# Performance work log

Hardware: AMD Instinct MI355X
Metric: run time of the kernel (lower is better)

Reference implementation:

```python
import jax, jax.numpy as jnp
import numpy as np

N_U, N_I, D, Q, NNZ, L = 100000, 100000, 64, 128, 3200000, 3
N = N_U + N_I

def setup_inputs() -> dict:
    key = jax.random.key(0)
    ks = jax.random.split(key, 9)
    user_emb = jax.random.normal(ks[0], (N_U, D), dtype=jnp.float32) * 0.1
    item_emb = jax.random.normal(ks[1], (N_I, D), dtype=jnp.float32) * 0.1
    adj_row = jax.random.randint(ks[2], (NNZ,), 0, N, dtype=jnp.int32)
    adj_col = jax.random.randint(ks[3], (NNZ,), 0, N, dtype=jnp.int32)
    # ~degree-normalized values so L-layer propagation stays stable
    adj_vals = jax.random.uniform(ks[4], (NNZ,), dtype=jnp.float32) / 16.0
    ut = jax.random.normal(ks[5], (Q, N_U), dtype=jnp.float32) * (1.0 / np.sqrt(N_U))
    vt = jax.random.normal(ks[6], (Q, N_I), dtype=jnp.float32) * (1.0 / np.sqrt(N_I))
    u_mul_s = jax.random.normal(ks[7], (N_U, Q), dtype=jnp.float32) * 0.1
    v_mul_s = jax.random.normal(ks[8], (N_I, Q), dtype=jnp.float32) * 0.1
    return {"user_emb": user_emb, "item_emb": item_emb, "adj_row": adj_row,
            "adj_col": adj_col, "adj_vals": adj_vals, "ut": ut, "vt": vt,
            "u_mul_s": u_mul_s, "v_mul_s": v_mul_s}

def _spmm(row, col, vals, x):
    # y[r] = sum_{e: row[e]==r} vals[e] * x[col[e]]
    return jax.ops.segment_sum(vals[:, None] * x[col], row, num_segments=N)

def reference(user_emb, item_emb, adj_row, adj_col, adj_vals, ut, vt, u_mul_s, v_mul_s):
    ego = jnp.concatenate([user_emb, item_emb], axis=0)  # [N, D]
    acc = jnp.zeros_like(ego)
    svd_u = jnp.zeros((N_U, D), dtype=ego.dtype)
    svd_i = jnp.zeros((N_I, D), dtype=ego.dtype)
    for _ in range(L):
        ego = _spmm(adj_row, adj_col, adj_vals, ego)
        acc = acc + ego
        ue, ie = ego[:N_U], ego[N_U:]
        ut_eu = ut @ ue            # [Q, D]
        vt_ei = vt @ ie            # [Q, D]
        svd_u = svd_u + u_mul_s @ vt_ei
        svd_i = svd_i + v_mul_s @ ut_eu
    mean = acc / L                 # mean over stacked layer embeddings
    return (mean[:N_U], svd_u, mean[N_U:], svd_i)
```

## Files before the change

kernel.cpp:

```cpp
#include <hip/hip_runtime.h>

constexpr int N_U  = 100000;
constexpr int N_I  = 100000;
constexpr int NTOT = 200000;
constexpr int D    = 64;
constexpr int Q    = 128;
constexpr int NNZ  = 3200000;
constexpr int SEG  = N_U * D;

constexpr int G1_CHUNK = 400;
constexpr int G1_NBLK  = 250;

constexpr int BROWS   = 512;
constexpr int NBUCK   = (NTOT + BROWS - 1) / BROWS;
constexpr int P_CHUNK = 8192;
constexpr int P_NBLK  = (NNZ + P_CHUNK - 1) / P_CHUNK;

constexpr int G2_ROWS = 64;
constexpr int G2_NBLK = (N_U + G2_ROWS - 1) / G2_ROWS;

__device__ __forceinline__ unsigned short f2bf(float f) {
  unsigned int b = __float_as_uint(f);
  return (unsigned short)((b + 0x7fff + ((b >> 16) & 1)) >> 16);
}
__device__ __forceinline__ float bf2f(unsigned short u) {
  return __uint_as_float((unsigned int)u << 16);
}

__global__ void __launch_bounds__(512) k_bhist(const int* __restrict__ row,
                                               int* __restrict__ part) {
  __shared__ int h[NBUCK];
  const int t = threadIdx.x;
  if (t < NBUCK) h[t] = 0;
  __syncthreads();
  const int e0 = blockIdx.x * P_CHUNK;
#pragma unroll
  for (int i = 0; i < P_CHUNK / 512; ++i) {
    int e = e0 + i * 512 + t;
    if (e < NNZ) atomicAdd(&h[row[e] >> 9], 1);
  }
  __syncthreads();
  if (t < NBUCK) part[blockIdx.x * NBUCK + t] = h[t];
}

__global__ void __launch_bounds__(512) k_bscan(int* __restrict__ part,
                                               int* __restrict__ outb,
                                               int* __restrict__ bbase) {
  __shared__ int s[512];
  const int t = threadIdx.x;
  int run = 0;
  if (t < NBUCK) {
    for (int blk = 0; blk < P_NBLK; ++blk) {
      int v = part[blk * NBUCK + t];
      outb[blk * NBUCK + t] = run;
      run += v;
    }
  }
  const int own = (t < NBUCK) ? run : 0;
  s[t] = own;
  __syncthreads();
  for (int off = 1; off < 512; off <<= 1) {
    int y = (t >= off) ? s[t - off] : 0;
    __syncthreads();
    s[t] += y;
    __syncthreads();
  }
  int excl = s[t] - own;
  if (t <= NBUCK) bbase[t] = excl;
}

__global__ void __launch_bounds__(512) k_mscat(const int* __restrict__ row,
                                               const int* __restrict__ col,
                                               const float* __restrict__ val,
                                               const int* __restrict__ outb,
                                               const int* __restrict__ bbase,
                                               int2* __restrict__ ebuck) {
  __shared__ int cur[NBUCK];
  const int t = threadIdx.x;
  if (t < NBUCK) cur[t] = bbase[t] + outb[blockIdx.x * NBUCK + t];
  __syncthreads();
  const int e0 = blockIdx.x * P_CHUNK;
#pragma unroll
  for (int i = 0; i < P_CHUNK / 512; ++i) {
    int e = e0 + i * 512 + t;
    if (e < NNZ) {
      int r = row[e];
      int b = r >> 9;
      int pos = atomicAdd(&cur[b], 1);
      ebuck[pos] = make_int2(col[e] | ((r & (BROWS - 1)) << 18), __float_as_int(val[e]));
    }
  }
}

__global__ void __launch_bounds__(512) k_rsort(const int* __restrict__ bbase,
                                               const int2* __restrict__ ebuck,
                                               int2* __restrict__ edges,
                                               int* __restrict__ rowptr) {
  __shared__ int s[512];
  __shared__ int cur[512];
  const int t = threadIdx.x;
  const int b = blockIdx.x;
  const int eb0 = bbase[b], eb1 = bbase[b + 1];
  cur[t] = 0;
  __syncthreads();
  for (int e = eb0 + t; e < eb1; e += 512) atomicAdd(&cur[ebuck[e].x >> 18], 1);
  __syncthreads();
  const int own = cur[t];
  s[t] = own;
  __syncthreads();
  for (int off = 1; off < 512; off <<= 1) {
    int y = (t >= off) ? s[t - off] : 0;
    __syncthreads();
    s[t] += y;
    __syncthreads();
  }
  const int excl = s[t] - own;
  const int r = (b << 9) + t;
  if (r < NTOT) rowptr[r] = eb0 + excl;
  if (b == NBUCK - 1 && t == 0) rowptr[NTOT] = NNZ;
  cur[t] = eb0 + excl;
  __syncthreads();
  for (int e = eb0 + t; e < eb1; e += 512) {
    int2 kv = ebuck[e];
    int pos = atomicAdd(&cur[kv.x >> 18], 1);
    edges[pos] = make_int2(kv.x & 0x3FFFF, kv.y);
  }
}

__global__ void k_cvt(const float* __restrict__ user_emb,
                      const float* __restrict__ item_emb,
                      unsigned short* __restrict__ e0) {
  int i = blockIdx.x * 256 + threadIdx.x;
  if (i >= NTOT * D / 8) return;
  size_t base = (size_t)i * 8;
  const float* src = (base < (size_t)SEG) ? (user_emb + base) : (item_emb + base - SEG);
  float4 v0 = *reinterpret_cast<const float4*>(src);
  float4 v1 = *reinterpret_cast<const float4*>(src + 4);
  union { unsigned short us[8]; uint4 u4; } pk;
  pk.us[0] = f2bf(v0.x); pk.us[1] = f2bf(v0.y); pk.us[2] = f2bf(v0.z); pk.us[3] = f2bf(v0.w);
  pk.us[4] = f2bf(v1.x); pk.us[5] = f2bf(v1.y); pk.us[6] = f2bf(v1.z); pk.us[7] = f2bf(v1.w);
  *reinterpret_cast<uint4*>(e0 + base) = pk.u4;
}

__global__ void k_spmm(const int* __restrict__ rowptr, const int2* __restrict__ edges,
                       const unsigned short* __restrict__ src,
                       unsigned short* __restrict__ dst) {
  const int r = (blockIdx.x * 256 + threadIdx.x) >> 6;
  const int lane = threadIdx.x & 63;
  if (r >= NTOT) return;
  const int e0 = rowptr[r], e1 = rowptr[r + 1];
  float sum = 0.f;
  int e = e0;
  for (; e + 8 <= e1; e += 8) {
    int2 d0 = edges[e + 0], d1 = edges[e + 1], d2 = edges[e + 2], d3 = edges[e + 3];
    int2 d4 = edges[e + 4], d5 = edges[e + 5], d6 = edges[e + 6], d7 = edges[e + 7];
    unsigned short u0 = src[((size_t)d0.x << 6) + lane];
    unsigned short u1 = src[((size_t)d1.x << 6) + lane];
    unsigned short u2 = src[((size_t)d2.x << 6) + lane];
    unsigned short u3 = src[((size_t)d3.x << 6) + lane];
    unsigned short u4 = src[((size_t)d4.x << 6) + lane];
    unsigned short u5 = src[((size_t)d5.x << 6) + lane];
    unsigned short u6 = src[((size_t)d6.x << 6) + lane];
    unsigned short u7 = src[((size_t)d7.x << 6) + lane];
    sum = fmaf(__int_as_float(d0.y), bf2f(u0), sum);
    sum = fmaf(__int_as_float(d1.y), bf2f(u1), sum);
    sum = fmaf(__int_as_float(d2.y), bf2f(u2), sum);
    sum = fmaf(__int_as_float(d3.y), bf2f(u3), sum);
    sum = fmaf(__int_as_float(d4.y), bf2f(u4), sum);
    sum = fmaf(__int_as_float(d5.y), bf2f(u5), sum);
    sum = fmaf(__int_as_float(d6.y), bf2f(u6), sum);
    sum = fmaf(__int_as_float(d7.y), bf2f(u7), sum);
  }
  for (; e + 2 <= e1; e += 2) {
    int2 d0 = edges[e + 0], d1 = edges[e + 1];
    unsigned short u0 = src[((size_t)d0.x << 6) + lane];
    unsigned short u1 = src[((size_t)d1.x << 6) + lane];
    sum = fmaf(__int_as_float(d0.y), bf2f(u0), sum);
    sum = fmaf(__int_as_float(d1.y), bf2f(u1), sum);
  }
  if (e < e1) {
    int2 d0 = edges[e];
    sum = fmaf(__int_as_float(d0.y), bf2f(src[((size_t)d0.x << 6) + lane]), sum);
  }
  dst[((size_t)r << 6) + lane] = f2bf(sum);
}

__global__ void k_mean(const unsigned short* __restrict__ e1,
                       const unsigned short* __restrict__ e2,
                       const unsigned short* __restrict__ e3,
                       float* __restrict__ mean_u, float* __restrict__ mean_i) {
  int i = blockIdx.x * 256 + threadIdx.x;
  if (i >= NTOT * D / 8) return;
  size_t base = (size_t)i * 8;
  uint4 a = *reinterpret_cast<const uint4*>(e1 + base);
  uint4 b = *reinterpret_cast<const uint4*>(e2 + base);
  uint4 c = *reinterpret_cast<const uint4*>(e3 + base);
  union { uint4 u4; unsigned short us[8]; } ua, ub, uc;
  ua.u4 = a; ub.u4 = b; uc.u4 = c;
  float o[8];
#pragma unroll
  for (int j = 0; j < 8; ++j)
    o[j] = (bf2f(ua.us[j]) + bf2f(ub.us[j]) + bf2f(uc.us[j])) * (1.f / 3.f);
  float* dstp = (base < (size_t)SEG) ? (mean_u + base) : (mean_i + base - SEG);
  *reinterpret_cast<float4*>(dstp) = make_float4(o[0], o[1], o[2], o[3]);
  *reinterpret_cast<float4*>(dstp + 4) = make_float4(o[4], o[5], o[6], o[7]);
}

__global__ void __launch_bounds__(512) k_g1(const float* __restrict__ ut,
                                            const float* __restrict__ vt,
                                            const float* __restrict__ accu,
                                            const float* __restrict__ acci,
                                            float* __restrict__ Ppart) {
  __shared__ float Wl[128 * 65];
  __shared__ float Xl[64 * 64];
  const int mat = blockIdx.y;
  const float* __restrict__ W = mat ? vt : ut;
  const float* __restrict__ X = mat ? acci : accu;
  const int t = threadIdx.x;
  const int q0 = (t >> 4) * 4;
  const int d0 = (t & 15) * 4;
  const int n0 = blockIdx.x * G1_CHUNK;
  const int n1 = min(n0 + G1_CHUNK, N_U);
  float4 a0 = {0, 0, 0, 0}, a1 = {0, 0, 0, 0}, a2 = {0, 0, 0, 0}, a3 = {0, 0, 0, 0};
  for (int k = n0; k < n1; k += 64) {
#pragma unroll
    for (int rep = 0; rep < 2; ++rep) {
      int f4 = t + rep * 512;
      int row = f4 >> 4;
      int c4 = (f4 & 15) * 4;
      int gr = k + row;
      float4 v = (gr < n1) ? *reinterpret_cast<const float4*>(X + (size_t)gr * 64 + c4)
                           : float4{0, 0, 0, 0};
      *reinterpret_cast<float4*>(&Xl[row * 64 + c4]) = v;
    }
    {
      int q = t >> 2;
      int c16 = (t & 3) * 16;
#pragma unroll
      for (int jj = 0; jj < 4; ++jj) {
        int kk = c16 + jj * 4;
        int gk = k + kk;
        float4 v = (gk < n1) ? *reinterpret_cast<const float4*>(W + (size_t)q * N_U + gk)
                             : float4{0, 0, 0, 0};
        *reinterpret_cast<float4*>(&Wl[q * 65 + kk]) = v;
      }
    }
    __syncthreads();
#pragma unroll 2
    for (int kk = 0; kk < 64; kk += 4) {
      float4 w0 = *reinterpret_cast<const float4*>(&Wl[(q0 + 0) * 65 + kk]);
      float4 w1 = *reinterpret_cast<const float4*>(&Wl[(q0 + 1) * 65 + kk]);
      float4 w2 = *reinterpret_cast<const float4*>(&Wl[(q0 + 2) * 65 + kk]);
      float4 w3 = *reinterpret_cast<const float4*>(&Wl[(q0 + 3) * 65 + kk]);
      float4 x0 = *reinterpret_cast<const float4*>(&Xl[(kk + 0) * 64 + d0]);
      float4 x1 = *reinterpret_cast<const float4*>(&Xl[(kk + 1) * 64 + d0]);
      float4 x2 = *reinterpret_cast<const float4*>(&Xl[(kk + 2) * 64 + d0]);
      float4 x3 = *reinterpret_cast<const float4*>(&Xl[(kk + 3) * 64 + d0]);
#define FMA16(aj, wj)                                                                 \
  aj.x = fmaf(wj.x, x0.x, aj.x); aj.y = fmaf(wj.x, x0.y, aj.y);                       \
  aj.z = fmaf(wj.x, x0.z, aj.z); aj.w = fmaf(wj.x, x0.w, aj.w);                       \
  aj.x = fmaf(wj.y, x1.x, aj.x); aj.y = fmaf(wj.y, x1.y, aj.y);                       \
  aj.z = fmaf(wj.y, x1.z, aj.z); aj.w = fmaf(wj.y, x1.w, aj.w);                       \
  aj.x = fmaf(wj.z, x2.x, aj.x); aj.y = fmaf(wj.z, x2.y, aj.y);                       \
  aj.z = fmaf(wj.z, x2.z, aj.z); aj.w = fmaf(wj.z, x2.w, aj.w);                       \
  aj.x = fmaf(wj.w, x3.x, aj.x); aj.y = fmaf(wj.w, x3.y, aj.y);                       \
  aj.z = fmaf(wj.w, x3.z, aj.z); aj.w = fmaf(wj.w, x3.w, aj.w);
      FMA16(a0, w0)
      FMA16(a1, w1)
      FMA16(a2, w2)
      FMA16(a3, w3)
#undef FMA16
    }
    __syncthreads();
  }
  float* dst = Ppart + ((size_t)mat * G1_NBLK + blockIdx.x) * (Q * D);
  *reinterpret_cast<float4*>(dst + (q0 + 0) * 64 + d0) = a0;
  *reinterpret_cast<float4*>(dst + (q0 + 1) * 64 + d0) = a1;
  *reinterpret_cast<float4*>(dst + (q0 + 2) * 64 + d0) = a2;
  *reinterpret_cast<float4*>(dst + (q0 + 3) * 64 + d0) = a3;
}

__global__ void k_reduce(const float* __restrict__ Ppart, float* __restrict__ P) {
  int idx = blockIdx.x * 256 + threadIdx.x;
  if (idx >= 2 * Q * D) return;
  int mat = idx >> 13;
  int qd = idx & (Q * D - 1);
  const float* src = Ppart + (size_t)mat * G1_NBLK * (Q * D) + qd;
  float s = 0.f;
#pragma unroll 4
  for (int b = 0; b < G1_NBLK; ++b) s += src[(size_t)b * (Q * D)];
  P[idx] = s * 3.f;
}

__global__ void __launch_bounds__(256) k_g2(const float* __restrict__ u_mul_s,
                                            const float* __restrict__ v_mul_s,
                                            const float* __restrict__ P,
                                            float* __restrict__ svd_u,
                                            float* __restrict__ svd_i) {
  __shared__ float Pl[Q * D];
  const int mat = blockIdx.y;
  const float* __restrict__ M  = mat ? v_mul_s : u_mul_s;
  const float* __restrict__ Pg = mat ? P : (P + Q * D);
  float* __restrict__ outp     = mat ? svd_i : svd_u;
  const int t = threadIdx.x;
#pragma unroll
  for (int i = 0; i < 8; ++i) {
    int idx = i * 256 + t;
    reinterpret_cast<float4*>(Pl)[idx] = reinterpret_cast<const float4*>(Pg)[idx];
  }
  __syncthreads();
  const int c0 = (t & 15) * 4;
  const int rbase = blockIdx.x * G2_ROWS + (t >> 4) * 4;
  const float4* mr0 = reinterpret_cast<const float4*>(M + (size_t)(rbase + 0 < N_U ? rbase + 0 : 0) * Q);
  const float4* mr1 = reinterpret_cast<const float4*>(M + (size_t)(rbase + 1 < N_U ? rbase + 1 : 0) * Q);
  const float4* mr2 = reinterpret_cast<const float4*>(M + (size_t)(rbase + 2 < N_U ? rbase + 2 : 0) * Q);
  const float4* mr3 = reinterpret_cast<const float4*>(M + (size_t)(rbase + 3 < N_U ? rbase + 3 : 0) * Q);
  float4 a0 = {0, 0, 0, 0}, a1 = {0, 0, 0, 0}, a2 = {0, 0, 0, 0}, a3 = {0, 0, 0, 0};
#pragma unroll 4
  for (int k4 = 0; k4 < Q / 4; ++k4) {
    float4 m0 = mr0[k4];
    float4 m1 = mr1[k4];
    float4 m2 = mr2[k4];
    float4 m3 = mr3[k4];
    float4 p0 = *reinterpret_cast<const float4*>(&Pl[(k4 * 4 + 0) * D + c0]);
    float4 p1 = *reinterpret_cast<const float4*>(&Pl[(k4 * 4 + 1) * D + c0]);
    float4 p2 = *reinterpret_cast<const float4*>(&Pl[(k4 * 4 + 2) * D + c0]);
    float4 p3 = *reinterpret_cast<const float4*>(&Pl[(k4 * 4 + 3) * D + c0]);
#define G2FMA(aj, mj)                                                                 \
  aj.x = fmaf(mj.x, p0.x, aj.x); aj.y = fmaf(mj.x, p0.y, aj.y);                       \
  aj.z = fmaf(mj.x, p0.z, aj.z); aj.w = fmaf(mj.x, p0.w, aj.w);                       \
  aj.x = fmaf(mj.y, p1.x, aj.x); aj.y = fmaf(mj.y, p1.y, aj.y);                       \
  aj.z = fmaf(mj.y, p1.z, aj.z); aj.w = fmaf(mj.y, p1.w, aj.w);                       \
  aj.x = fmaf(mj.z, p2.x, aj.x); aj.y = fmaf(mj.z, p2.y, aj.y);                       \
  aj.z = fmaf(mj.z, p2.z, aj.z); aj.w = fmaf(mj.z, p2.w, aj.w);                       \
  aj.x = fmaf(mj.w, p3.x, aj.x); aj.y = fmaf(mj.w, p3.y, aj.y);                       \
  aj.z = fmaf(mj.w, p3.z, aj.z); aj.w = fmaf(mj.w, p3.w, aj.w);
    G2FMA(a0, m0)
    G2FMA(a1, m1)
    G2FMA(a2, m2)
    G2FMA(a3, m3)
#undef G2FMA
  }
  if (rbase + 0 < N_U) *reinterpret_cast<float4*>(outp + (size_t)(rbase + 0) * D + c0) = a0;
  if (rbase + 1 < N_U) *reinterpret_cast<float4*>(outp + (size_t)(rbase + 1) * D + c0) = a1;
  if (rbase + 2 < N_U) *reinterpret_cast<float4*>(outp + (size_t)(rbase + 2) * D + c0) = a2;
  if (rbase + 3 < N_U) *reinterpret_cast<float4*>(outp + (size_t)(rbase + 3) * D + c0) = a3;
}

extern "C" void kernel_launch(void* const* d_in, const int* in_sizes, int n_in,
                              void* d_out, int out_size, void* d_ws, size_t ws_size,
                              hipStream_t stream) {
  const float* user_emb = (const float*)d_in[0];
  const float* item_emb = (const float*)d_in[1];
  const int*   adj_row  = (const int*)d_in[2];
  const int*   adj_col  = (const int*)d_in[3];
  const float* adj_vals = (const float*)d_in[4];
  const float* ut       = (const float*)d_in[5];
  const float* vt       = (const float*)d_in[6];
  const float* u_mul_s  = (const float*)d_in[7];
  const float* v_mul_s  = (const float*)d_in[8];
  float* out = (float*)d_out;

  char* ws = (char*)d_ws;
  size_t off = 0;
  auto alloc = [&](size_t bytes) -> void* {
    void* p = ws + off;
    off = (off + bytes + 255) & ~(size_t)255;
    return p;
  };
  unsigned short* eb0 = (unsigned short*)alloc((size_t)NTOT * D * 2);
  unsigned short* eb1 = (unsigned short*)alloc((size_t)NTOT * D * 2);
  unsigned short* eb2 = (unsigned short*)alloc((size_t)NTOT * D * 2);
  unsigned short* eb3 = (unsigned short*)alloc((size_t)NTOT * D * 2);
  int2*  ebuck  = (int2*)alloc((size_t)NNZ * 8);
  int2*  edges  = (int2*)alloc((size_t)NNZ * 8);
  int*   rowptr = (int*)alloc((size_t)(NTOT + 1) * 4);
  int*   part   = (int*)alloc((size_t)P_NBLK * NBUCK * 4);
  int*   outb   = (int*)alloc((size_t)P_NBLK * NBUCK * 4);
  int*   bbase  = (int*)alloc((size_t)(NBUCK + 1) * 4);
  float* P      = (float*)alloc(2 * Q * D * 4);
  float* Ppart  = (float*)alloc((size_t)2 * G1_NBLK * Q * D * 4);

  float* mean_u = out;
  float* svd_u  = out + (size_t)SEG;
  float* mean_i = out + 2 * (size_t)SEG;
  float* svd_i  = out + 3 * (size_t)SEG;

  k_bhist<<<P_NBLK, 512, 0, stream>>>(adj_row, part);
  k_bscan<<<1, 512, 0, stream>>>(part, outb, bbase);
  k_mscat<<<P_NBLK, 512, 0, stream>>>(adj_row, adj_col, adj_vals, outb, bbase, ebuck);
  k_rsort<<<NBUCK, 512, 0, stream>>>(bbase, ebuck, edges, rowptr);

  k_cvt<<<(NTOT * D / 8 + 255) / 256, 256, 0, stream>>>(user_emb, item_emb, eb0);

  const int spmmGrid = (NTOT * 64) / 256;
  k_spmm<<<spmmGrid, 256, 0, stream>>>(rowptr, edges, eb0, eb1);
  k_spmm<<<spmmGrid, 256, 0, stream>>>(rowptr, edges, eb1, eb2);
  k_spmm<<<spmmGrid, 256, 0, stream>>>(rowptr, edges, eb2, eb3);

  k_mean<<<(NTOT * D / 8 + 255) / 256, 256, 0, stream>>>(eb1, eb2, eb3, mean_u, mean_i);

  k_g1<<<dim3(G1_NBLK, 2), 512, 0, stream>>>(ut, vt, mean_u, mean_i, Ppart);
  k_reduce<<<(2 * Q * D + 255) / 256, 256, 0, stream>>>(Ppart, P);

  k_g2<<<dim3(G2_NBLK, 2), 256, 0, stream>>>(u_mul_s, v_mul_s, P, svd_u, svd_i);
}
```

Before: 660.5 us.

## Fuse conversion into histogram, parallelize bucket scan, fold mean into last SpMM

The bf16 conversion of the embeddings now runs as extra blocks of the histogram kernel, which saves a launch. The serial per-bucket scan is split into a parallel wave-level scan per bucket plus a small global scan. The SpMM unrolls 16 edges with two accumulators, uses 32-bit indexing and nontemporal stores. The third layer computes the layer mean directly, so the separate mean kernel and one bf16 buffer are no longer needed. This cuts launch count and one full pass over the embeddings, at the cost of more register pressure in the SpMM.

```diff
diff --git a/kernel.cpp b/kernel.cpp
--- a/kernel.cpp
+++ b/kernel.cpp
@@ -19,6 +19,9 @@
 constexpr int G2_ROWS = 64;
 constexpr int G2_NBLK = (N_U + G2_ROWS - 1) / G2_ROWS;
 
+constexpr int CVT_CNT  = NTOT * D / 8;
+constexpr int CVT_BLKS = (CVT_CNT + 511) / 512;
+
 __device__ __forceinline__ unsigned short f2bf(float f) {
   unsigned int b = __float_as_uint(f);
   return (unsigned short)((b + 0x7fff + ((b >> 16) & 1)) >> 16);
@@ -27,36 +30,65 @@
   return __uint_as_float((unsigned int)u << 16);
 }
 
-__global__ void __launch_bounds__(512) k_bhist(const int* __restrict__ row,
-                                               int* __restrict__ part) {
+__global__ void __launch_bounds__(512) k_pre(const int* __restrict__ row,
+                                             int* __restrict__ part,
+                                             const float* __restrict__ user_emb,
+                                             const float* __restrict__ item_emb,
+                                             unsigned short* __restrict__ e0) {
   __shared__ int h[NBUCK];
   const int t = threadIdx.x;
-  if (t < NBUCK) h[t] = 0;
-  __syncthreads();
-  const int e0 = blockIdx.x * P_CHUNK;
-#pragma unroll
-  for (int i = 0; i < P_CHUNK / 512; ++i) {
-    int e = e0 + i * 512 + t;
-    if (e < NNZ) atomicAdd(&h[row[e] >> 9], 1);
-  }
-  __syncthreads();
-  if (t < NBUCK) part[blockIdx.x * NBUCK + t] = h[t];
-}
-
-__global__ void __launch_bounds__(512) k_bscan(int* __restrict__ part,
+  if (blockIdx.x < (unsigned)P_NBLK) {
+    if (t < NBUCK) h[t] = 0;
+    __syncthreads();
+    const int e0i = blockIdx.x * P_CHUNK;
+#pragma unroll
+    for (int i = 0; i < P_CHUNK / 512; ++i) {
+      int e = e0i + i * 512 + t;
+      if (e < NNZ) atomicAdd(&h[row[e] >> 9], 1);
+    }
+    __syncthreads();
+    if (t < NBUCK) part[blockIdx.x * NBUCK + t] = h[t];
+  } else {
+    int i = (blockIdx.x - P_NBLK) * 512 + t;
+    if (i >= CVT_CNT) return;
+    size_t base = (size_t)i * 8;
+    const float* src = (base < (size_t)SEG) ? (user_emb + base) : (item_emb + base - SEG);
+    float4 v0 = *reinterpret_cast<const float4*>(src);
+    float4 v1 = *reinterpret_cast<const float4*>(src + 4);
+    union { unsigned short us[8]; uint4 u4; } pk;
+    pk.us[0] = f2bf(v0.x); pk.us[1] = f2bf(v0.y); pk.us[2] = f2bf(v0.z); pk.us[3] = f2bf(v0.w);
+    pk.us[4] = f2bf(v1.x); pk.us[5] = f2bf(v1.y); pk.us[6] = f2bf(v1.z); pk.us[7] = f2bf(v1.w);
+    *reinterpret_cast<uint4*>(e0 + base) = pk.u4;
+  }
+}
+
+__global__ void __launch_bounds__(64) k_bscanA(const int* __restrict__ part,
                                                int* __restrict__ outb,
-                                               int* __restrict__ bbase) {
+                                               int* __restrict__ btot) {
+  const int b = blockIdx.x;
+  const int l = threadIdx.x;
+  int carry = 0;
+#pragma unroll
+  for (int round = 0; round < (P_NBLK + 63) / 64; ++round) {
+    int blk = round * 64 + l;
+    int v = (blk < P_NBLK) ? part[blk * NBUCK + b] : 0;
+    int x = v;
+#pragma unroll
+    for (int off = 1; off < 64; off <<= 1) {
+      int y = __shfl_up(x, off, 64);
+      if (l >= off) x += y;
+    }
+    if (blk < P_NBLK) outb[blk * NBUCK + b] = carry + x - v;
+    carry += __shfl(x, 63, 64);
+  }
+  if (l == 0) btot[b] = carry;
+}
+
+__global__ void __launch_bounds__(512) k_bscanB(const int* __restrict__ btot,
+                                                int* __restrict__ bbase) {
   __shared__ int s[512];
   const int t = threadIdx.x;
-  int run = 0;
-  if (t < NBUCK) {
-    for (int blk = 0; blk < P_NBLK; ++blk) {
-      int v = part[blk * NBUCK + t];
-      outb[blk * NBUCK + t] = run;
-      run += v;
-    }
-  }
-  const int own = (t < NBUCK) ? run : 0;
+  const int own = (t < NBUCK) ? btot[t] : 0;
   s[t] = own;
   __syncthreads();
   for (int off = 1; off < 512; off <<= 1) {
@@ -65,8 +97,7 @@
     s[t] += y;
     __syncthreads();
   }
-  int excl = s[t] - own;
-  if (t <= NBUCK) bbase[t] = excl;
+  if (t <= NBUCK) bbase[t] = s[t] - own;
 }
 
 __global__ void __launch_bounds__(512) k_mscat(const int* __restrict__ row,
@@ -127,83 +158,68 @@
   }
 }
 
-__global__ void k_cvt(const float* __restrict__ user_emb,
-                      const float* __restrict__ item_emb,
-                      unsigned short* __restrict__ e0) {
-  int i = blockIdx.x * 256 + threadIdx.x;
-  if (i >= NTOT * D / 8) return;
-  size_t base = (size_t)i * 8;
-  const float* src = (base < (size_t)SEG) ? (user_emb + base) : (item_emb + base - SEG);
-  float4 v0 = *reinterpret_cast<const float4*>(src);
-  float4 v1 = *reinterpret_cast<const float4*>(src + 4);
-  union { unsigned short us[8]; uint4 u4; } pk;
-  pk.us[0] = f2bf(v0.x); pk.us[1] = f2bf(v0.y); pk.us[2] = f2bf(v0.z); pk.us[3] = f2bf(v0.w);
-  pk.us[4] = f2bf(v1.x); pk.us[5] = f2bf(v1.y); pk.us[6] = f2bf(v1.z); pk.us[7] = f2bf(v1.w);
-  *reinterpret_cast<uint4*>(e0 + base) = pk.u4;
-}
-
+template <int FINAL>
 __global__ void k_spmm(const int* __restrict__ rowptr, const int2* __restrict__ edges,
                        const unsigned short* __restrict__ src,
-                       unsigned short* __restrict__ dst) {
+                       unsigned short* __restrict__ dst,
+                       const unsigned short* __restrict__ p1,
+                       const unsigned short* __restrict__ p2,
+                       float* __restrict__ mean_u, float* __restrict__ mean_i) {
   const int r = (blockIdx.x * 256 + threadIdx.x) >> 6;
   const int lane = threadIdx.x & 63;
   if (r >= NTOT) return;
-  const int e0 = rowptr[r], e1 = rowptr[r + 1];
-  float sum = 0.f;
-  int e = e0;
-  for (; e + 8 <= e1; e += 8) {
+  const int eb = rowptr[r], ee = rowptr[r + 1];
+  float sA = 0.f, sB = 0.f;
+  int e = eb;
+#define GIDX(dd) ((unsigned)(((dd).x << 6) + lane))
+  for (; e + 16 <= ee; e += 16) {
     int2 d0 = edges[e + 0], d1 = edges[e + 1], d2 = edges[e + 2], d3 = edges[e + 3];
     int2 d4 = edges[e + 4], d5 = edges[e + 5], d6 = edges[e + 6], d7 = edges[e + 7];
-    unsigned short u0 = src[((size_t)d0.x << 6) + lane];
-    unsigned short u1 = src[((size_t)d1.x << 6) + lane];
-    unsigned short u2 = src[((size_t)d2.x << 6) + lane];
-    unsigned short u3 = src[((size_t)d3.x << 6) + lane];
-    unsigned short u4 = src[((size_t)d4.x << 6) + lane];
-    unsigned short u5 = src[((size_t)d5.x << 6) + lane];
-    unsigned short u6 = src[((size_t)d6.x << 6) + lane];
-    unsigned short u7 = src[((size_t)d7.x << 6) + lane];
-    sum = fmaf(__int_as_float(d0.y), bf2f(u0), sum);
-    sum = fmaf(__int_as_float(d1.y), bf2f(u1), sum);
-    sum = fmaf(__int_as_float(d2.y), bf2f(u2), sum);
-    sum = fmaf(__int_as_float(d3.y), bf2f(u3), sum);
-    sum = fmaf(__int_as_float(d4.y), bf2f(u4), sum);
-    sum = fmaf(__int_as_float(d5.y), bf2f(u5), sum);
-    sum = fmaf(__int_as_float(d6.y), bf2f(u6), sum);
-    sum = fmaf(__int_as_float(d7.y), bf2f(u7), sum);
-  }
-  for (; e + 2 <= e1; e += 2) {
-    int2 d0 = edges[e + 0], d1 = edges[e + 1];
-    unsigned short u0 = src[((size_t)d0.x << 6) + lane];
-    unsigned short u1 = src[((size_t)d1.x << 6) + lane];
-    sum = fmaf(__int_as_float(d0.y), bf2f(u0), sum);
-    sum = fmaf(__int_as_float(d1.y), bf2f(u1), sum);
-  }
-  if (e < e1) {
+    int2 d8 = edges[e + 8], d9 = edges[e + 9], da = edges[e + 10], db = edges[e + 11];
+    int2 dc = edges[e + 12], dd = edges[e + 13], de = edges[e + 14], df = edges[e + 15];
+    unsigned short u0 = src[GIDX(d0)], u1 = src[GIDX(d1)], u2 = src[GIDX(d2)], u3 = src[GIDX(d3)];
+    unsigned short u4 = src[GIDX(d4)], u5 = src[GIDX(d5)], u6 = src[GIDX(d6)], u7 = src[GIDX(d7)];
+    unsigned short u8 = src[GIDX(d8)], u9 = src[GIDX(d9)], ua = src[GIDX(da)], ub = src[GIDX(db)];
+    unsigned short uc = src[GIDX(dc)], ud = src[GIDX(dd)], ue = src[GIDX(de)], uf = src[GIDX(df)];
+    sA = fmaf(__int_as_float(d0.y), bf2f(u0), sA);
+    sB = fmaf(__int_as_float(d1.y), bf2f(u1), sB);
+    sA = fmaf(__int_as_float(d2.y), bf2f(u2), sA);
+    sB = fmaf(__int_as_float(d3.y), bf2f(u3), sB);
+    sA = fmaf(__int_as_float(d4.y), bf2f(u4), sA);
+    sB = fmaf(__int_as_float(d5.y), bf2f(u5), sB);
+    sA = fmaf(__int_as_float(d6.y), bf2f(u6), sA);
+    sB = fmaf(__int_as_float(d7.y), bf2f(u7), sB);
+    sA = fmaf(__int_as_float(d8.y), bf2f(u8), sA);
+    sB = fmaf(__int_as_float(d9.y), bf2f(u9), sB);
+    sA = fmaf(__int_as_float(da.y), bf2f(ua), sA);
+    sB = fmaf(__int_as_float(db.y), bf2f(ub), sB);
+    sA = fmaf(__int_as_float(dc.y), bf2f(uc), sA);
+    sB = fmaf(__int_as_float(dd.y), bf2f(ud), sB);
+    sA = fmaf(__int_as_float(de.y), bf2f(ue), sA);
+    sB = fmaf(__int_as_float(df.y), bf2f(uf), sB);
+  }
+  for (; e + 4 <= ee; e += 4) {
+    int2 d0 = edges[e + 0], d1 = edges[e + 1], d2 = edges[e + 2], d3 = edges[e + 3];
+    unsigned short u0 = src[GIDX(d0)], u1 = src[GIDX(d1)], u2 = src[GIDX(d2)], u3 = src[GIDX(d3)];
+    sA = fmaf(__int_as_float(d0.y), bf2f(u0), sA);
+    sB = fmaf(__int_as_float(d1.y), bf2f(u1), sB);
+    sA = fmaf(__int_as_float(d2.y), bf2f(u2), sA);
+    sB = fmaf(__int_as_float(d3.y), bf2f(u3), sB);
+  }
+  for (; e < ee; ++e) {
     int2 d0 = edges[e];
-    sum = fmaf(__int_as_float(d0.y), bf2f(src[((size_t)d0.x << 6) + lane]), sum);
-  }
-  dst[((size_t)r << 6) + lane] = f2bf(sum);
-}
-
-__global__ void k_mean(const unsigned short* __restrict__ e1,
-                       const unsigned short* __restrict__ e2,
-                       const unsigned short* __restrict__ e3,
-                       float* __restrict__ mean_u, float* __restrict__ mean_i) {
-  int i = blockIdx.x * 256 + threadIdx.x;
-  if (i >= NTOT * D / 8) return;
-  size_t base = (size_t)i * 8;
-  uint4 a = *reinterpret_cast<const uint4*>(e1 + base);
-  uint4 b = *reinterpret_cast<const uint4*>(e2 + base);
-  uint4 c = *reinterpret_cast<const uint4*>(e3 + base);
-  union { uint4 u4; unsigned short us[8]; } ua, ub, uc;
-  ua.u4 = a; ub.u4 = b; uc.u4 = c;
-  float o[8];
-#pragma unroll
-  for (int j = 0; j < 8; ++j)
-    o[j] = (bf2f(ua.us[j]) + bf2f(ub.us[j]) + bf2f(uc.us[j])) * (1.f / 3.f);
-  float* dstp = (base < (size_t)SEG) ? (mean_u + base) : (mean_i + base - SEG);
-  *reinterpret_cast<float4*>(dstp) = make_float4(o[0], o[1], o[2], o[3]);
-  *reinterpret_cast<float4*>(dstp + 4) = make_float4(o[4], o[5], o[6], o[7]);
+    sA = fmaf(__int_as_float(d0.y), bf2f(src[GIDX(d0)]), sA);
+  }
+#undef GIDX
+  const float sum = sA + sB;
+  const unsigned idx = ((unsigned)r << 6) + lane;
+  if (!FINAL) {
+    __builtin_nontemporal_store(f2bf(sum), &dst[idx]);
+  } else {
+    float m = (bf2f(p1[idx]) + bf2f(p2[idx]) + sum) * (1.f / 3.f);
+    if (r < N_U) mean_u[idx] = m;
+    else         mean_i[idx - (unsigned)SEG] = m;
+  }
 }
 
 __global__ void __launch_bounds__(512) k_g1(const float* __restrict__ ut,
@@ -371,12 +387,12 @@
   unsigned short* eb0 = (unsigned short*)alloc((size_t)NTOT * D * 2);
   unsigned short* eb1 = (unsigned short*)alloc((size_t)NTOT * D * 2);
   unsigned short* eb2 = (unsigned short*)alloc((size_t)NTOT * D * 2);
-  unsigned short* eb3 = (unsigned short*)alloc((size_t)NTOT * D * 2);
   int2*  ebuck  = (int2*)alloc((size_t)NNZ * 8);
   int2*  edges  = (int2*)alloc((size_t)NNZ * 8);
   int*   rowptr = (int*)alloc((size_t)(NTOT + 1) * 4);
   int*   part   = (int*)alloc((size_t)P_NBLK * NBUCK * 4);
   int*   outb   = (int*)alloc((size_t)P_NBLK * NBUCK * 4);
+  int*   btot   = (int*)alloc((size_t)NBUCK * 4);
   int*   bbase  = (int*)alloc((size_t)(NBUCK + 1) * 4);
   float* P      = (float*)alloc(2 * Q * D * 4);
   float* Ppart  = (float*)alloc((size_t)2 * G1_NBLK * Q * D * 4);
@@ -386,19 +402,19 @@
   float* mean_i = out + 2 * (size_t)SEG;
   float* svd_i  = out + 3 * (size_t)SEG;
 
-  k_bhist<<<P_NBLK, 512, 0, stream>>>(adj_row, part);
-  k_bscan<<<1, 512, 0, stream>>>(part, outb, bbase);
+  k_pre<<<P_NBLK + CVT_BLKS, 512, 0, stream>>>(adj_row, part, user_emb, item_emb, eb0);
+  k_bscanA<<<NBUCK, 64, 0, stream>>>(part, outb, btot);
+  k_bscanB<<<1, 512, 0, stream>>>(btot, bbase);
   k_mscat<<<P_NBLK, 512, 0, stream>>>(adj_row, adj_col, adj_vals, outb, bbase, ebuck);
   k_rsort<<<NBUCK, 512, 0, stream>>>(bbase, ebuck, edges, rowptr);
 
-  k_cvt<<<(NTOT * D / 8 + 255) / 256, 256, 0, stream>>>(user_emb, item_emb, eb0);
-
   const int spmmGrid = (NTOT * 64) / 256;
-  k_spmm<<<spmmGrid, 256, 0, stream>>>(rowptr, edges, eb0, eb1);
-  k_spmm<<<spmmGrid, 256, 0, stream>>>(rowptr, edges, eb1, eb2);
-  k_spmm<<<spmmGrid, 256, 0, stream>>>(rowptr, edges, eb2, eb3);
-
-  k_mean<<<(NTOT * D / 8 + 255) / 256, 256, 0, stream>>>(eb1, eb2, eb3, mean_u, mean_i);
+  k_spmm<0><<<spmmGrid, 256, 0, stream>>>(rowptr, edges, eb0, eb1, nullptr, nullptr,
+                                          nullptr, nullptr);
+  k_spmm<0><<<spmmGrid, 256, 0, stream>>>(rowptr, edges, eb1, eb2, nullptr, nullptr,
+                                          nullptr, nullptr);
+  k_spmm<1><<<spmmGrid, 256, 0, stream>>>(rowptr, edges, eb2, nullptr, eb1, eb2,
+                                          mean_u, mean_i);
 
   k_g1<<<dim3(G1_NBLK, 2), 512, 0, stream>>>(ut, vt, mean_u, mean_i, Ppart);
   k_reduce<<<(2 * Q * D + 255) / 256, 256, 0, stream>>>(Ppart, P);
```

After: 635.8 us. 1.04x faster.
